# Performance work log

Hardware: AMD Instinct MI355X
Metric: run time of the kernel (lower is better)

The kernel has to match this reference:

```python
import jax, jax.numpy as jnp
import numpy as np

LABELS_NUM_COUNT = [500000, 120000, 80000, 45000, 30000, 250000, 15000, 9000,
                    60000, 7000, 180000, 22000, 11000, 95000, 5000, 40000]
B, W = 2097152, 16  # batch, num_classes


def _build_penalty_matrix():
    c = np.asarray(LABELS_NUM_COUNT, dtype=np.float32)
    P = np.maximum(c[:, None], c[None, :]) / (c[:, None] + c[None, :])
    np.fill_diagonal(P, 1.0)
    return jnp.asarray(P)  # [W, W]


def setup_inputs() -> dict:
    key = jax.random.key(0)
    k1, k2 = jax.random.split(key)
    predict = jax.random.normal(k1, (B, W), dtype=jnp.float32)
    target = jax.random.normal(k2, (B, W), dtype=jnp.float32)
    return {"predict": predict, "target": target,
            "penalty_matrix": _build_penalty_matrix()}


def reference(predict, target, penalty_matrix):
    # `logpredict` in the original is actually softmax(predict).
    probs = jax.nn.softmax(predict, axis=-1)              # [B, W]
    pre = jnp.argmax(predict, axis=-1)                    # [B] predicted class
    tar = jnp.argmax(target, axis=-1)                     # [B] target class
    # scatter_ writes 1 at the predicted slot, then the loop overwrites it with
    # penalty[tar, pre] on mismatch or 0 on match -> net weight is:
    w = jnp.where(pre == tar, jnp.float32(0.0), penalty_matrix[tar, pre])  # [B]
    # sum(onehot * probs, -1) == probs at the predicted class
    p_at_pre = jnp.take_along_axis(probs, pre[:, None], axis=-1)[:, 0]     # [B]
    return jnp.mean(w * p_at_pre)
```

## Files before the change

### kernel.cpp

```cpp
#include <hip/hip_runtime.h>

#define NROWS 2097152
#define W 16

__global__ __launch_bounds__(256) void cel_weight_kernel(
    const float* __restrict__ predict,
    const float* __restrict__ target,
    const float* __restrict__ penalty,
    float* __restrict__ out)
{
    __shared__ float s_pen[W * W];
    __shared__ float s_part[4];

    const int tid = threadIdx.x;
    if (tid < W * W) s_pen[tid] = penalty[tid];
    __syncthreads();

    float acc = 0.0f;
    const int stride = gridDim.x * blockDim.x;

    for (int r = blockIdx.x * blockDim.x + tid; r < NROWS; r += stride) {
        const float4* prow = (const float4*)(predict + (size_t)r * W);
        const float4* trow = (const float4*)(target + (size_t)r * W);
        float4 p0 = prow[0], p1 = prow[1], p2 = prow[2], p3 = prow[3];
        float4 t0 = trow[0], t1 = trow[1], t2 = trow[2], t3 = trow[3];

        float pv[W] = {p0.x, p0.y, p0.z, p0.w, p1.x, p1.y, p1.z, p1.w,
                       p2.x, p2.y, p2.z, p2.w, p3.x, p3.y, p3.z, p3.w};
        float tv[W] = {t0.x, t0.y, t0.z, t0.w, t1.x, t1.y, t1.z, t1.w,
                       t2.x, t2.y, t2.z, t2.w, t3.x, t3.y, t3.z, t3.w};

        float pmax = pv[0]; int pidx = 0;
        #pragma unroll
        for (int j = 1; j < W; ++j) {
            if (pv[j] > pmax) { pmax = pv[j]; pidx = j; }
        }
        float s = 0.0f;
        #pragma unroll
        for (int j = 0; j < W; ++j) s += __expf(pv[j] - pmax);

        float tmax = tv[0]; int tidx = 0;
        #pragma unroll
        for (int j = 1; j < W; ++j) {
            if (tv[j] > tmax) { tmax = tv[j]; tidx = j; }
        }

        float wgt = (pidx == tidx) ? 0.0f : s_pen[tidx * W + pidx];
        acc += wgt / s;
    }

    #pragma unroll
    for (int off = 32; off > 0; off >>= 1)
        acc += __shfl_down(acc, off);

    const int lane = tid & 63;
    const int wid  = tid >> 6;
    if (lane == 0) s_part[wid] = acc;
    __syncthreads();

    if (tid == 0) {
        float tot = s_part[0] + s_part[1] + s_part[2] + s_part[3];
        atomicAdd(out, tot * (1.0f / (float)NROWS));
    }
}

extern "C" void kernel_launch(void* const* d_in, const int* in_sizes, int n_in,
                              void* d_out, int out_size, void* d_ws, size_t ws_size,
                              hipStream_t stream)
{
    const float* predict = (const float*)d_in[0];
    const float* target  = (const float*)d_in[1];
    const float* penalty = (const float*)d_in[2];
    float* out = (float*)d_out;

    hipMemsetAsync(out, 0, sizeof(float) * out_size, stream);

    dim3 grid(2048), block(256);
    cel_weight_kernel<<<grid, block, 0, stream>>>(predict, target, penalty, out);
}
```

Measured before the change: 274.0 us.

## Use one row per thread with swizzled blocks and two-pass partial reduction

Replaces the grid-stride loop over 2048 blocks with one block per 256 rows (8192 blocks), each thread handling a single row. Block indices are swizzled across 8 groups, and loads use nontemporal hints. The global float atomicAdd and the memset are replaced by per-block partials written to workspace plus a second single-block reduce kernel. This aims to expose more memory parallelism and remove atomic contention, at the cost of an extra kernel launch and more block scheduling overhead.

```diff
diff --git a/kernel.cpp b/kernel.cpp
--- a/kernel.cpp
+++ b/kernel.cpp
@@ -1,53 +1,62 @@
 #include <hip/hip_runtime.h>
 
-#define NROWS 2097152
-#define W 16
+#define NROWS    2097152
+#define W        16
+#define NTHREADS 256
+#define NBLK     (NROWS / NTHREADS)
+
+typedef float f4 __attribute__((ext_vector_type(4)));
 
 __global__ __launch_bounds__(256) void cel_weight_kernel(
     const float* __restrict__ predict,
     const float* __restrict__ target,
     const float* __restrict__ penalty,
-    float* __restrict__ out)
+    float* __restrict__ partials)
 {
     __shared__ float s_pen[W * W];
     __shared__ float s_part[4];
 
     const int tid = threadIdx.x;
-    if (tid < W * W) s_pen[tid] = penalty[tid];
+    s_pen[tid] = penalty[tid];
     __syncthreads();
 
-    float acc = 0.0f;
-    const int stride = gridDim.x * blockDim.x;
+    const int bid = (int)blockIdx.x;
+    const int sw  = (bid & 7) * (NBLK / 8) + (bid >> 3);
+    const int row = sw * NTHREADS + tid;
 
-    for (int r = blockIdx.x * blockDim.x + tid; r < NROWS; r += stride) {
-        const float4* prow = (const float4*)(predict + (size_t)r * W);
-        const float4* trow = (const float4*)(target + (size_t)r * W);
-        float4 p0 = prow[0], p1 = prow[1], p2 = prow[2], p3 = prow[3];
-        float4 t0 = trow[0], t1 = trow[1], t2 = trow[2], t3 = trow[3];
+    const f4* prow = (const f4*)(predict + (size_t)row * W);
+    const f4* trow = (const f4*)(target  + (size_t)row * W);
 
-        float pv[W] = {p0.x, p0.y, p0.z, p0.w, p1.x, p1.y, p1.z, p1.w,
-                       p2.x, p2.y, p2.z, p2.w, p3.x, p3.y, p3.z, p3.w};
-        float tv[W] = {t0.x, t0.y, t0.z, t0.w, t1.x, t1.y, t1.z, t1.w,
-                       t2.x, t2.y, t2.z, t2.w, t3.x, t3.y, t3.z, t3.w};
+    f4 p0 = __builtin_nontemporal_load(prow + 0);
+    f4 p1 = __builtin_nontemporal_load(prow + 1);
+    f4 p2 = __builtin_nontemporal_load(prow + 2);
+    f4 p3 = __builtin_nontemporal_load(prow + 3);
+    f4 t0 = __builtin_nontemporal_load(trow + 0);
+    f4 t1 = __builtin_nontemporal_load(trow + 1);
+    f4 t2 = __builtin_nontemporal_load(trow + 2);
+    f4 t3 = __builtin_nontemporal_load(trow + 3);
 
-        float pmax = pv[0]; int pidx = 0;
-        #pragma unroll
-        for (int j = 1; j < W; ++j) {
-            if (pv[j] > pmax) { pmax = pv[j]; pidx = j; }
-        }
-        float s = 0.0f;
-        #pragma unroll
-        for (int j = 0; j < W; ++j) s += __expf(pv[j] - pmax);
+    float pv[W] = {p0.x, p0.y, p0.z, p0.w, p1.x, p1.y, p1.z, p1.w,
+                   p2.x, p2.y, p2.z, p2.w, p3.x, p3.y, p3.z, p3.w};
+    float tv[W] = {t0.x, t0.y, t0.z, t0.w, t1.x, t1.y, t1.z, t1.w,
+                   t2.x, t2.y, t2.z, t2.w, t3.x, t3.y, t3.z, t3.w};
 
-        float tmax = tv[0]; int tidx = 0;
-        #pragma unroll
-        for (int j = 1; j < W; ++j) {
-            if (tv[j] > tmax) { tmax = tv[j]; tidx = j; }
-        }
+    float pmax = pv[0]; int pidx = 0;
+    #pragma unroll
+    for (int j = 1; j < W; ++j)
+        if (pv[j] > pmax) { pmax = pv[j]; pidx = j; }
 
-        float wgt = (pidx == tidx) ? 0.0f : s_pen[tidx * W + pidx];
-        acc += wgt / s;
-    }
+    float s = 0.0f;
+    #pragma unroll
+    for (int j = 0; j < W; ++j) s += __expf(pv[j] - pmax);
+
+    float tmax = tv[0]; int tidx = 0;
+    #pragma unroll
+    for (int j = 1; j < W; ++j)
+        if (tv[j] > tmax) { tmax = tv[j]; tidx = j; }
+
+    float wgt = (pidx == tidx) ? 0.0f : s_pen[tidx * W + pidx];
+    float acc = wgt / s;
 
     #pragma unroll
     for (int off = 32; off > 0; off >>= 1)
@@ -57,11 +66,26 @@
     const int wid  = tid >> 6;
     if (lane == 0) s_part[wid] = acc;
     __syncthreads();
+    if (tid == 0)
+        partials[bid] = s_part[0] + s_part[1] + s_part[2] + s_part[3];
+}
 
-    if (tid == 0) {
-        float tot = s_part[0] + s_part[1] + s_part[2] + s_part[3];
-        atomicAdd(out, tot * (1.0f / (float)NROWS));
-    }
+__global__ __launch_bounds__(256) void reduce_kernel(
+    const float* __restrict__ partials, float* __restrict__ out)
+{
+    __shared__ float sp[4];
+    const int tid = threadIdx.x;
+    float a = 0.0f;
+    #pragma unroll
+    for (int i = 0; i < NBLK / NTHREADS; ++i)
+        a += partials[tid + i * NTHREADS];
+    #pragma unroll
+    for (int off = 32; off > 0; off >>= 1)
+        a += __shfl_down(a, off);
+    if ((tid & 63) == 0) sp[tid >> 6] = a;
+    __syncthreads();
+    if (tid == 0)
+        out[0] = (sp[0] + sp[1] + sp[2] + sp[3]) * (1.0f / (float)NROWS);
 }
 
 extern "C" void kernel_launch(void* const* d_in, const int* in_sizes, int n_in,
@@ -71,10 +95,10 @@
     const float* predict = (const float*)d_in[0];
     const float* target  = (const float*)d_in[1];
     const float* penalty = (const float*)d_in[2];
-    float* out = (float*)d_out;
+    float* out      = (float*)d_out;
+    float* partials = (float*)d_ws;
 
-    hipMemsetAsync(out, 0, sizeof(float) * out_size, stream);
-
-    dim3 grid(2048), block(256);
-    cel_weight_kernel<<<grid, block, 0, stream>>>(predict, target, penalty, out);
+    cel_weight_kernel<<<dim3(NBLK), dim3(NTHREADS), 0, stream>>>(
+        predict, target, penalty, partials);
+    reduce_kernel<<<dim3(1), dim3(NTHREADS), 0, stream>>>(partials, out);
 }
```

Measured after the change: 284.4 us. 3.8% more time.
